# Performance work log

Hardware: AMD Instinct MI355X
Metric: run time of the kernel (lower is better)

The kernel has to match this reference:

```python
import jax, jax.numpy as jnp
import numpy as np

KERNEL_SIZE = 4
SCALE = 0.5


def setup_inputs() -> dict:
    key = jax.random.key(0)
    k1, k2, k3 = jax.random.split(key, 3)
    M, K, N = 16384, 1024, 4096
    x = jax.random.normal(k1, (M, K), dtype=jnp.float32)
    weight = jax.random.normal(k2, (N, K), dtype=jnp.float32)
    bias = jax.random.normal(k3, (N,), dtype=jnp.float32)
    return {"x": x, "weight": weight, "bias": bias}


def reference(x, weight, bias):
    # y = x @ W^T + b : (M, N)
    y = jnp.einsum('mk,nk->mn', x, weight) + bias[None, :]
    M, N = y.shape
    valid_n = (N // KERNEL_SIZE) * KERNEL_SIZE
    # MaxPool1d(kernel_size, stride=kernel_size): (M, N//k, k) -> max over window
    pooled = jnp.max(y[:, :valid_n].reshape(M, valid_n // KERNEL_SIZE, KERNEL_SIZE), axis=-1)
    # sum over pooled features, then scale -> (M,)
    return jnp.sum(pooled, axis=-1) * SCALE
```

## Files before the change

### kernel.cpp

```cpp
#include <hip/hip_runtime.h>
#include <stdint.h>

#define M_DIM 16384
#define K_DIM 1024
#define N_DIM 4096
#define BM 128
#define BN 128
#define LDSP 40

#define TILE_ELEMS (128 * K_DIM)
#define SLAB_ELEMS (128 * 32)
#define NSLAB_X ((M_DIM / 128) * 32)
#define NSLAB_W ((N_DIM / 128) * 32)

typedef __bf16 bf16;
typedef __attribute__((ext_vector_type(8))) __bf16 bf16x8;
typedef __attribute__((ext_vector_type(4))) float f32x4;

__device__ __forceinline__ uint32_t pack2_bf16(float a, float b) {
    uint32_t ua = __float_as_uint(a);
    uint32_t ub = __float_as_uint(b);
    ua += 0x7fffu + ((ua >> 16) & 1u);
    ub += 0x7fffu + ((ub >> 16) & 1u);
    return (ua >> 16) | (ub & 0xffff0000u);
}

__global__ __launch_bounds__(256) void convert_pack_kernel(
    const float* __restrict__ x, const float* __restrict__ w,
    bf16* __restrict__ xp, bf16* __restrict__ wp)
{
    int slab = blockIdx.x;
    const float* src;
    bf16* dst;
    if (slab < NSLAB_X) { src = x; dst = xp; }
    else                { slab -= NSLAB_X; src = w; dst = wp; }
    const int tile = slab >> 5;
    const int s    = slab & 31;

    __shared__ uint32_t ls[128 * 16];

    const int t = threadIdx.x;
    {
        const int r  = t >> 1;
        const int kh = (t & 1) * 16;
        const float4* p = (const float4*)(src + (size_t)(tile * 128 + r) * K_DIM + s * 32 + kh);
        float4 a = p[0], b = p[1], c = p[2], d = p[3];
        uint32_t* lrow = &ls[r * 16 + (kh >> 1)];
        lrow[0] = pack2_bf16(a.x, a.y);
        lrow[1] = pack2_bf16(a.z, a.w);
        lrow[2] = pack2_bf16(b.x, b.y);
        lrow[3] = pack2_bf16(b.z, b.w);
        lrow[4] = pack2_bf16(c.x, c.y);
        lrow[5] = pack2_bf16(c.z, c.w);
        lrow[6] = pack2_bf16(d.x, d.y);
        lrow[7] = pack2_bf16(d.z, d.w);
    }
    __syncthreads();
    uint4* dst4 = (uint4*)(dst + (size_t)tile * TILE_ELEMS + (size_t)s * SLAB_ELEMS);
    #pragma unroll
    for (int p = 0; p < 2; ++p) {
        const int c   = t + p * 256;
        const int lane = c & 63;
        const int rb   = c >> 6;
        const int q    = lane >> 4;
        const int lrow = lane & 15;
        const int r    = rb * 16 + lrow;
        const uint32_t* lp = &ls[r * 16 + q * 4];
        uint4 v;
        v.x = lp[0]; v.y = lp[1]; v.z = lp[2]; v.w = lp[3];
        dst4[c] = v;
    }
}

__global__ __launch_bounds__(256) void gemm_pool_direct_kernel(
    const bf16* __restrict__ xp, const bf16* __restrict__ wp,
    const float* __restrict__ bias, float* __restrict__ out)
{
    const int bx = blockIdx.x;
    const int by = blockIdx.y;

    const int lane = threadIdx.x & 63;
    const int wave = threadIdx.x >> 6;
    const int wm = wave >> 1;
    const int wn = wave & 1;
    const int lr = lane & 15;
    const int quad = lane >> 4;

    const bf16* Abase = xp + (size_t)by * TILE_ELEMS + (wm * 4) * 512 + lane * 8;
    const bf16* Bbase = wp + (size_t)bx * TILE_ELEMS + (wn * 4) * 512 + lane * 8;

    f32x4 acc[4][4] = {};

    #pragma unroll 2
    for (int s = 0; s < 32; ++s) {
        const bf16* ga = Abase + s * SLAB_ELEMS;
        const bf16* gb = Bbase + s * SLAB_ELEMS;
        bf16x8 af[4], bfr[4];
        #pragma unroll
        for (int i = 0; i < 4; ++i) af[i]  = *(const bf16x8*)(ga + i * 512);
        #pragma unroll
        for (int j = 0; j < 4; ++j) bfr[j] = *(const bf16x8*)(gb + j * 512);
        #pragma unroll
        for (int i = 0; i < 4; ++i)
            #pragma unroll
            for (int j = 0; j < 4; ++j)
                acc[i][j] = __builtin_amdgcn_mfma_f32_16x16x32_bf16(af[i], bfr[j], acc[i][j], 0, 0, 0);
    }

    float bv[4];
    #pragma unroll
    for (int j = 0; j < 4; ++j)
        bv[j] = bias[bx * BN + wn * 64 + j * 16 + lr];

    #pragma unroll
    for (int i = 0; i < 4; ++i) {
        float rs[4] = {0.f, 0.f, 0.f, 0.f};
        #pragma unroll
        for (int j = 0; j < 4; ++j) {
            #pragma unroll
            for (int r = 0; r < 4; ++r) {
                float t = acc[i][j][r] + bv[j];
                t = fmaxf(t, __shfl_xor(t, 1, 64));
                t = fmaxf(t, __shfl_xor(t, 2, 64));
                rs[r] += t;
            }
        }
        #pragma unroll
        for (int r = 0; r < 4; ++r) {
            rs[r] += __shfl_xor(rs[r], 4, 64);
            rs[r] += __shfl_xor(rs[r], 8, 64);
        }
        if (lr == 0) {
            const int row = by * BM + wm * 64 + i * 16 + quad * 4;
            #pragma unroll
            for (int r = 0; r < 4; ++r)
                atomicAdd(&out[row + r], rs[r] * 0.5f);
        }
    }
}

__global__ __launch_bounds__(256) void fused_linear_pool_kernel(
    const float* __restrict__ x, const float* __restrict__ wt,
    const float* __restrict__ bias, float* __restrict__ out)
{
    __shared__ uint32_t sA[BM * LDSP / 2];
    __shared__ uint32_t sB[BN * LDSP / 2];

    const int tid = threadIdx.x;
    const int bx = blockIdx.x;
    const int by = blockIdx.y;

    const float* Abase = x  + (size_t)by * BM * K_DIM;
    const float* Bbase = wt + (size_t)bx * BN * K_DIM;

    const int lane = tid & 63;
    const int wave = tid >> 6;
    const int wm = wave >> 1;
    const int wn = wave & 1;
    const int lr = lane & 15;
    const int quad = lane >> 4;

    const int srow  = tid >> 2;
    const int scol  = (tid & 3) * 8;
    const int swidx = (tid & 3) * 4;

    f32x4 acc[4][4] = {};

    for (int kt = 0; kt < K_DIM; kt += 32) {
        #pragma unroll
        for (int p = 0; p < 2; ++p) {
            const int r = srow + p * 64;
            const float4* ga = (const float4*)(Abase + (size_t)r * K_DIM + kt + scol);
            const float4* gb = (const float4*)(Bbase + (size_t)r * K_DIM + kt + scol);
            float4 a0 = ga[0], a1 = ga[1], b0 = gb[0], b1 = gb[1];
            uint4 wa;
            wa.x = pack2_bf16(a0.x, a0.y); wa.y = pack2_bf16(a0.z, a0.w);
            wa.z = pack2_bf16(a1.x, a1.y); wa.w = pack2_bf16(a1.z, a1.w);
            *(uint4*)&sA[r * (LDSP / 2) + swidx] = wa;
            uint4 wbv;
            wbv.x = pack2_bf16(b0.x, b0.y); wbv.y = pack2_bf16(b0.z, b0.w);
            wbv.z = pack2_bf16(b1.x, b1.y); wbv.w = pack2_bf16(b1.z, b1.w);
            *(uint4*)&sB[r * (LDSP / 2) + swidx] = wbv;
        }
        __syncthreads();

        bf16x8 af[4], bfr[4];
        #pragma unroll
        for (int i = 0; i < 4; ++i)
            af[i] = *(const bf16x8*)((const bf16*)sA + (wm * 64 + i * 16 + lr) * LDSP + quad * 8);
        #pragma unroll
        for (int j = 0; j < 4; ++j)
            bfr[j] = *(const bf16x8*)((const bf16*)sB + (wn * 64 + j * 16 + lr) * LDSP + quad * 8);

        #pragma unroll
        for (int i = 0; i < 4; ++i)
            #pragma unroll
            for (int j = 0; j < 4; ++j)
                acc[i][j] = __builtin_amdgcn_mfma_f32_16x16x32_bf16(af[i], bfr[j], acc[i][j], 0, 0, 0);
        __syncthreads();
    }

    float bv[4];
    #pragma unroll
    for (int j = 0; j < 4; ++j)
        bv[j] = bias[bx * BN + wn * 64 + j * 16 + lr];

    #pragma unroll
    for (int i = 0; i < 4; ++i) {
        float rsum[4] = {0.f, 0.f, 0.f, 0.f};
        #pragma unroll
        for (int j = 0; j < 4; ++j) {
            #pragma unroll
            for (int r = 0; r < 4; ++r) {
                float t = acc[i][j][r] + bv[j];
                t = fmaxf(t, __shfl_xor(t, 1, 64));
                t = fmaxf(t, __shfl_xor(t, 2, 64));
                t += __shfl_xor(t, 4, 64);
                t += __shfl_xor(t, 8, 64);
                rsum[r] += t;
            }
        }
        if (lr == 0) {
            const int row = by * BM + wm * 64 + i * 16 + quad * 4;
            #pragma unroll
            for (int r = 0; r < 4; ++r)
                atomicAdd(&out[row + r], rsum[r] * 0.5f);
        }
    }
}

extern "C" void kernel_launch(void* const* d_in, const int* in_sizes, int n_in,
                              void* d_out, int out_size, void* d_ws, size_t ws_size,
                              hipStream_t stream) {
    const float* x  = (const float*)d_in[0];
    const float* wt = (const float*)d_in[1];
    const float* bs = (const float*)d_in[2];
    float* out = (float*)d_out;

    hipMemsetAsync(out, 0, (size_t)out_size * sizeof(float), stream);

    const size_t xe = (size_t)M_DIM * K_DIM;
    const size_t we = (size_t)N_DIM * K_DIM;
    const size_t need = (xe + we) * sizeof(bf16);

    dim3 grid(N_DIM / BN, M_DIM / BM);

    if (ws_size >= need) {
        bf16* xp = (bf16*)d_ws;
        bf16* wp = xp + xe;
        convert_pack_kernel<<<NSLAB_X + NSLAB_W, 256, 0, stream>>>(x, wt, xp, wp);
        gemm_pool_direct_kernel<<<grid, 256, 0, stream>>>(xp, wp, bs, out);
    } else {
        fused_linear_pool_kernel<<<grid, 256, 0, stream>>>(x, wt, bs, out);
    }
}
```

Before: 295.5 us.

## Double-buffer fragment loads, remap block order, pad convert LDS rows

The GEMM main loop now prefetches the next K-slab's fragments into a second register set while the MFMAs for the current slab run, so global load latency can overlap compute. The launch becomes a 1-D grid whose block index is remapped so that consecutive blocks share the same weight tile and spread across X tiles, which is meant to improve L2 reuse across XCDs. The convert kernel pads its LDS rows and uses 128-bit LDS stores and loads to cut bank conflicts and instruction count. The extra register buffers raise VGPR pressure and may lower occupancy.

```diff
diff --git a/kernel.cpp b/kernel.cpp
--- a/kernel.cpp
+++ b/kernel.cpp
@@ -12,6 +12,7 @@
 #define SLAB_ELEMS (128 * 32)
 #define NSLAB_X ((M_DIM / 128) * 32)
 #define NSLAB_W ((N_DIM / 128) * 32)
+#define CROW 20
 
 typedef __bf16 bf16;
 typedef __attribute__((ext_vector_type(8))) __bf16 bf16x8;
@@ -37,7 +38,7 @@
     const int tile = slab >> 5;
     const int s    = slab & 31;
 
-    __shared__ uint32_t ls[128 * 16];
+    __shared__ uint32_t ls[128 * CROW];
 
     const int t = threadIdx.x;
     {
@@ -45,39 +46,53 @@
         const int kh = (t & 1) * 16;
         const float4* p = (const float4*)(src + (size_t)(tile * 128 + r) * K_DIM + s * 32 + kh);
         float4 a = p[0], b = p[1], c = p[2], d = p[3];
-        uint32_t* lrow = &ls[r * 16 + (kh >> 1)];
-        lrow[0] = pack2_bf16(a.x, a.y);
-        lrow[1] = pack2_bf16(a.z, a.w);
-        lrow[2] = pack2_bf16(b.x, b.y);
-        lrow[3] = pack2_bf16(b.z, b.w);
-        lrow[4] = pack2_bf16(c.x, c.y);
-        lrow[5] = pack2_bf16(c.z, c.w);
-        lrow[6] = pack2_bf16(d.x, d.y);
-        lrow[7] = pack2_bf16(d.z, d.w);
+        uint4* lp = (uint4*)&ls[r * CROW + (t & 1) * 8];
+        uint4 v0, v1;
+        v0.x = pack2_bf16(a.x, a.y); v0.y = pack2_bf16(a.z, a.w);
+        v0.z = pack2_bf16(b.x, b.y); v0.w = pack2_bf16(b.z, b.w);
+        v1.x = pack2_bf16(c.x, c.y); v1.y = pack2_bf16(c.z, c.w);
+        v1.z = pack2_bf16(d.x, d.y); v1.w = pack2_bf16(d.z, d.w);
+        lp[0] = v0; lp[1] = v1;
     }
     __syncthreads();
     uint4* dst4 = (uint4*)(dst + (size_t)tile * TILE_ELEMS + (size_t)s * SLAB_ELEMS);
     #pragma unroll
     for (int p = 0; p < 2; ++p) {
-        const int c   = t + p * 256;
+        const int c    = t + p * 256;
         const int lane = c & 63;
         const int rb   = c >> 6;
         const int q    = lane >> 4;
         const int lrow = lane & 15;
         const int r    = rb * 16 + lrow;
-        const uint32_t* lp = &ls[r * 16 + q * 4];
-        uint4 v;
-        v.x = lp[0]; v.y = lp[1]; v.z = lp[2]; v.w = lp[3];
-        dst4[c] = v;
-    }
+        const uint4* lp = (const uint4*)&ls[r * CROW + q * 4];
+        dst4[c] = lp[0];
+    }
+}
+
+__device__ __forceinline__ void load_frags(const bf16* ga, const bf16* gb,
+                                           bf16x8* af, bf16x8* bf) {
+    #pragma unroll
+    for (int i = 0; i < 4; ++i) af[i] = *(const bf16x8*)(ga + i * 512);
+    #pragma unroll
+    for (int j = 0; j < 4; ++j) bf[j] = *(const bf16x8*)(gb + j * 512);
+}
+
+__device__ __forceinline__ void do_mfma(const bf16x8* af, const bf16x8* bf,
+                                        f32x4 acc[4][4]) {
+    #pragma unroll
+    for (int i = 0; i < 4; ++i)
+        #pragma unroll
+        for (int j = 0; j < 4; ++j)
+            acc[i][j] = __builtin_amdgcn_mfma_f32_16x16x32_bf16(af[i], bf[j], acc[i][j], 0, 0, 0);
 }
 
 __global__ __launch_bounds__(256) void gemm_pool_direct_kernel(
     const bf16* __restrict__ xp, const bf16* __restrict__ wp,
     const float* __restrict__ bias, float* __restrict__ out)
 {
-    const int bx = blockIdx.x;
-    const int by = blockIdx.y;
+    const int b  = blockIdx.x;
+    const int by = (b & 7) * 16 + ((b >> 3) & 15);
+    const int bx = b >> 7;
 
     const int lane = threadIdx.x & 63;
     const int wave = threadIdx.x >> 6;
@@ -90,21 +105,16 @@
     const bf16* Bbase = wp + (size_t)bx * TILE_ELEMS + (wn * 4) * 512 + lane * 8;
 
     f32x4 acc[4][4] = {};
-
-    #pragma unroll 2
-    for (int s = 0; s < 32; ++s) {
-        const bf16* ga = Abase + s * SLAB_ELEMS;
-        const bf16* gb = Bbase + s * SLAB_ELEMS;
-        bf16x8 af[4], bfr[4];
-        #pragma unroll
-        for (int i = 0; i < 4; ++i) af[i]  = *(const bf16x8*)(ga + i * 512);
-        #pragma unroll
-        for (int j = 0; j < 4; ++j) bfr[j] = *(const bf16x8*)(gb + j * 512);
-        #pragma unroll
-        for (int i = 0; i < 4; ++i)
-            #pragma unroll
-            for (int j = 0; j < 4; ++j)
-                acc[i][j] = __builtin_amdgcn_mfma_f32_16x16x32_bf16(af[i], bfr[j], acc[i][j], 0, 0, 0);
+    bf16x8 aA[4], bA[4], aB[4], bB[4];
+
+    load_frags(Abase, Bbase, aA, bA);
+    #pragma unroll
+    for (int s = 0; s < 32; s += 2) {
+        load_frags(Abase + (s + 1) * SLAB_ELEMS, Bbase + (s + 1) * SLAB_ELEMS, aB, bB);
+        do_mfma(aA, bA, acc);
+        if (s + 2 < 32)
+            load_frags(Abase + (s + 2) * SLAB_ELEMS, Bbase + (s + 2) * SLAB_ELEMS, aA, bA);
+        do_mfma(aB, bB, acc);
     }
 
     float bv[4];
@@ -243,14 +253,13 @@
     const size_t we = (size_t)N_DIM * K_DIM;
     const size_t need = (xe + we) * sizeof(bf16);
 
-    dim3 grid(N_DIM / BN, M_DIM / BM);
-
     if (ws_size >= need) {
         bf16* xp = (bf16*)d_ws;
         bf16* wp = xp + xe;
         convert_pack_kernel<<<NSLAB_X + NSLAB_W, 256, 0, stream>>>(x, wt, xp, wp);
-        gemm_pool_direct_kernel<<<grid, 256, 0, stream>>>(xp, wp, bs, out);
+        gemm_pool_direct_kernel<<<(M_DIM / BM) * (N_DIM / BN), 256, 0, stream>>>(xp, wp, bs, out);
     } else {
+        dim3 grid(N_DIM / BN, M_DIM / BM);
         fused_linear_pool_kernel<<<grid, 256, 0, stream>>>(x, wt, bs, out);
     }
 }
```

New measurement: 270.7 us. -8.4%, faster.
